# Optimization experiments

Measured on AMD Instinct MI355X. Metric: run time of the kernel, lower is better.

The kernel has to match this reference:

```python
import jax, jax.numpy as jnp
import numpy as np

HEADS = 4
HIDDEN = 128
NEG_SLOPE = 0.2
BN_EPS = 1e-5


def setup_inputs() -> dict:
    key = jax.random.key(0)
    ks = jax.random.split(key, 10)
    N, E, C, H = 10000, 320000, HIDDEN, HEADS
    D = C  # out_channels per head == hidden_channels
    glorot = lambda k, shape, fan: jax.random.normal(k, shape, dtype=jnp.float32) * np.float32(np.sqrt(2.0 / fan))
    x = jax.random.normal(ks[0], (N, C), dtype=jnp.float32)
    edge_index = jax.random.randint(ks[1], (2, E), 0, N, dtype=jnp.int64)
    W_l = glorot(ks[2], (C, H * D), C + H * D)
    b_l = jnp.zeros((H * D,), dtype=jnp.float32)
    W_r = glorot(ks[3], (C, H * D), C + H * D)
    b_r = jnp.zeros((H * D,), dtype=jnp.float32)
    att = glorot(ks[4], (H, D), D)
    bias = jnp.zeros((D,), dtype=jnp.float32)
    gamma = jnp.ones((D,), dtype=jnp.float32)
    beta = jnp.zeros((D,), dtype=jnp.float32)
    return {"x": x, "edge_index": edge_index, "W_l": W_l, "b_l": b_l,
            "W_r": W_r, "b_r": b_r, "att": att, "bias": bias,
            "gamma": gamma, "beta": beta}


def reference(x, edge_index, W_l, b_l, W_r, b_r, att, bias, gamma, beta):
    N, C = x.shape
    H = HEADS
    D = C
    # add self loops (PyG default add_self_loops=True)
    loops = jnp.arange(N, dtype=edge_index.dtype)
    src = jnp.concatenate([edge_index[0], loops])  # [E+N]
    dst = jnp.concatenate([edge_index[1], loops])  # [E+N]
    # GATv2: separate source/target transforms (share_weights=False)
    xl = (x @ W_l + b_l).reshape(N, H, D)  # source-side features
    xr = (x @ W_r + b_r).reshape(N, H, D)  # target-side features
    # per-edge score: a^T LeakyReLU(xl_j + xr_i)
    m = jax.nn.leaky_relu(xl[src] + xr[dst], negative_slope=NEG_SLOPE)  # [E',H,D]
    e = jnp.einsum('ehd,hd->eh', m, att)  # [E',H]
    # segment softmax over destination nodes
    emax = jax.ops.segment_max(e, dst, num_segments=N)  # [N,H]
    ee = jnp.exp(e - emax[dst])
    denom = jax.ops.segment_sum(ee, dst, num_segments=N)  # [N,H]
    alpha = ee / (denom[dst] + 1e-16)  # [E',H]
    # aggregate: sum_j alpha_ij * xl_j
    out = jax.ops.segment_sum(alpha[..., None] * xl[src], dst, num_segments=N)  # [N,H,D]
    out = out.mean(axis=1) + bias  # concat=False -> mean over heads, then bias
    # BatchNorm1d (training-mode batch statistics) + ReLU; dropout p=0
    mu = out.mean(axis=0)
    var = out.var(axis=0)
    out = gamma * (out - mu) * jax.lax.rsqrt(var + BN_EPS) + beta
    return jax.nn.relu(out)
```

## Files before the change

kernel.cpp:

```cpp
#include <hip/hip_runtime.h>
#include <math.h>

#define HEADS 4
#define HD 512
#define NEG 0.2f

typedef __attribute__((ext_vector_type(8))) short bf16x8;
typedef __attribute__((ext_vector_type(4))) float f32x4;

__device__ __forceinline__ unsigned short f2b(float f) {
    unsigned u = __float_as_uint(f);
    unsigned r = (u + 0x7fff + ((u >> 16) & 1)) >> 16;
    return (unsigned short)r;
}
__device__ __forceinline__ float lo16(unsigned u) { return __uint_as_float(u << 16); }
__device__ __forceinline__ float hi16(unsigned u) { return __uint_as_float(u & 0xffff0000u); }

__global__ __launch_bounds__(256) void prologue1(
    const float* __restrict__ Wl, const float* __restrict__ Wr,
    unsigned short* __restrict__ wlt, unsigned short* __restrict__ wrt,
    const int* __restrict__ ei, int E, int* __restrict__ deg,
    int* __restrict__ pos)
{
    const int bid = blockIdx.x;
    const int tid = threadIdx.x;
    if (bid < 128) {
        __shared__ float t[32][33];
        const int bx = bid & 15, by = (bid >> 4) & 3, bz = bid >> 6;
        const float* W = bz ? Wr : Wl;
        unsigned short* Wt = bz ? wrt : wlt;
        const int c0 = bx * 32, k0 = by * 32;
        {
            int k = tid >> 3, c4 = (tid & 7) * 4;
            float4 v = *(const float4*)(W + (size_t)(k0 + k) * 512 + c0 + c4);
            t[k][c4] = v.x; t[k][c4 + 1] = v.y; t[k][c4 + 2] = v.z; t[k][c4 + 3] = v.w;
        }
        __syncthreads();
        {
            int c = tid >> 3, k4 = (tid & 7) * 4;
            ushort4 o;
            o.x = f2b(t[k4][c]); o.y = f2b(t[k4 + 1][c]);
            o.z = f2b(t[k4 + 2][c]); o.w = f2b(t[k4 + 3][c]);
            *(ushort4*)(Wt + (size_t)(c0 + c) * 128 + k0 + k4) = o;
        }
    } else {
        int e = (bid - 128) * 256 + tid;
        if (e < E) pos[e] = atomicAdd(&deg[ei[E + e]], 1);
    }
}

__global__ __launch_bounds__(256) void scan_rowstart(
    const int* __restrict__ deg, int* __restrict__ rowstart, int N)
{
    __shared__ int ssum[256];
    int tid = threadIdx.x;
    int chunk = (N + 255) / 256;
    int start = tid * chunk;
    int end = min(start + chunk, N);
    int s = 0;
    for (int i = start; i < end; ++i) s += deg[i];
    ssum[tid] = s;
    __syncthreads();
    if (tid == 0) {
        int acc = 0;
        for (int i = 0; i < 256; ++i) { int t = ssum[i]; ssum[i] = acc; acc += t; }
    }
    __syncthreads();
    int acc = ssum[tid];
    for (int i = start; i < end; ++i) { rowstart[i] = acc; acc += deg[i]; }
    if (tid == 255) rowstart[N] = acc;
}

__global__ __launch_bounds__(256) void prologue2(
    const float* __restrict__ x,
    const unsigned short* __restrict__ wlt, const unsigned short* __restrict__ wrt,
    const float* __restrict__ bl, const float* __restrict__ br,
    unsigned short* __restrict__ xlb, unsigned short* __restrict__ xrb, int N,
    const int* __restrict__ ei, int E, const int* __restrict__ rowstart,
    const int* __restrict__ pos, int* __restrict__ adj)
{
    const int nrb = (N + 63) / 64;
    const int bid = blockIdx.x;
    if (bid >= nrb * 8) {
        int e = (bid - nrb * 8) * 256 + threadIdx.x;
        if (e < E) {
            int src = ei[e], dst = ei[E + e];
            adj[rowstart[dst] + pos[e]] = src;
        }
        return;
    }
    __shared__ float tile[4][16][132];

    const int bx = bid >> 3, by = bid & 7;
    const int wv = threadIdx.x >> 6;
    const int lane = threadIdx.x & 63;
    const int wsel = by >> 2;
    const int cb0 = (by & 3) * 128;
    const unsigned short* Wt = wsel ? wrt : wlt;
    const float* bias = wsel ? br : bl;
    unsigned short* out = wsel ? xrb : xlb;

    const int r0 = bx * 64 + wv * 16;
    const int row16 = lane & 15;
    const int kg = lane >> 4;
    int ar = r0 + row16;
    int arc = (ar < N) ? ar : (N - 1);
    const float* xrow = x + (size_t)arc * 128;

    f32x4 acc[8];
    #pragma unroll
    for (int i = 0; i < 8; ++i) acc[i] = (f32x4){0.f, 0.f, 0.f, 0.f};

    #pragma unroll
    for (int ks = 0; ks < 4; ++ks) {
        float4 f0 = *(const float4*)(xrow + ks * 32 + kg * 8);
        float4 f1 = *(const float4*)(xrow + ks * 32 + kg * 8 + 4);
        bf16x8 a;
        a[0] = f2b(f0.x); a[1] = f2b(f0.y); a[2] = f2b(f0.z); a[3] = f2b(f0.w);
        a[4] = f2b(f1.x); a[5] = f2b(f1.y); a[6] = f2b(f1.z); a[7] = f2b(f1.w);
        #pragma unroll
        for (int cb = 0; cb < 8; ++cb) {
            int col = cb0 + cb * 16 + row16;
            bf16x8 b = *(const bf16x8*)(Wt + (size_t)col * 128 + ks * 32 + kg * 8);
            acc[cb] = __builtin_amdgcn_mfma_f32_16x16x32_bf16(a, b, acc[cb], 0, 0, 0);
        }
    }

    #pragma unroll
    for (int cb = 0; cb < 8; ++cb) {
        int c = cb * 16 + row16;
        #pragma unroll
        for (int r = 0; r < 4; ++r)
            tile[wv][kg * 4 + r][c] = acc[cb][r];
    }
    __syncthreads();

    #pragma unroll
    for (int p = 0; p < 4; ++p) {
        int row = p * 4 + (lane >> 4);
        int grow = r0 + row;
        if (grow < N) {
            int c8 = (lane & 15) * 8;
            float4 b0v = *(const float4*)(bias + cb0 + c8);
            float4 b1v = *(const float4*)(bias + cb0 + c8 + 4);
            const float* tp = &tile[wv][row][c8];
            unsigned short t0 = f2b(tp[0] + b0v.x), t1 = f2b(tp[1] + b0v.y);
            unsigned short t2 = f2b(tp[2] + b0v.z), t3 = f2b(tp[3] + b0v.w);
            unsigned short t4 = f2b(tp[4] + b1v.x), t5 = f2b(tp[5] + b1v.y);
            unsigned short t6 = f2b(tp[6] + b1v.z), t7 = f2b(tp[7] + b1v.w);
            uint4 u;
            u.x = (unsigned)t0 | ((unsigned)t1 << 16);
            u.y = (unsigned)t2 | ((unsigned)t3 << 16);
            u.z = (unsigned)t4 | ((unsigned)t5 << 16);
            u.w = (unsigned)t6 | ((unsigned)t7 << 16);
            *(uint4*)(out + (size_t)grow * 512 + cb0 + c8) = u;
        }
    }
}

__global__ __launch_bounds__(256) void gat_aggr(
    const unsigned short* __restrict__ xlb, const unsigned short* __restrict__ xrb,
    const float* __restrict__ att, const float* __restrict__ bias,
    const int* __restrict__ rowstart, const int* __restrict__ adj,
    float* __restrict__ outm, int N)
{
    const int dst = blockIdx.x;
    const int wv = threadIdx.x >> 6;
    const int lane = threadIdx.x & 63;
    const int off = lane * 8;

    __shared__ float accs[4][64][9];

    uint4 ur = *(const uint4*)(xrb + (size_t)dst * HD + off);
    float xrv[8] = {lo16(ur.x), hi16(ur.x), lo16(ur.y), hi16(ur.y),
                    lo16(ur.z), hi16(ur.z), lo16(ur.w), hi16(ur.w)};
    const float4* pa = (const float4*)(att + off);
    float4 a0 = pa[0], a1 = pa[1];
    float av[8]  = {a0.x, a0.y, a0.z, a0.w, a1.x, a1.y, a1.z, a1.w};

    float dsum0 = 0.f, dsum1 = 0.f;
    float acc0[8] = {0.f, 0.f, 0.f, 0.f, 0.f, 0.f, 0.f, 0.f};
    float acc1[8] = {0.f, 0.f, 0.f, 0.f, 0.f, 0.f, 0.f, 0.f};

    auto proc = [&](int src, float& dsum, float* acc) {
        uint4 u = *(const uint4*)(xlb + (size_t)src * HD + off);
        float xlv[8] = {lo16(u.x), hi16(u.x), lo16(u.y), hi16(u.y),
                        lo16(u.z), hi16(u.z), lo16(u.w), hi16(u.w)};
        float s = 0.f;
        #pragma unroll
        for (int j = 0; j < 8; ++j) {
            float v = xlv[j] + xrv[j];
            s = fmaf(fmaxf(v, NEG * v), av[j], s);
        }
        s += __shfl_xor(s, 1, 64);
        s += __shfl_xor(s, 2, 64);
        s += __shfl_xor(s, 4, 64);
        s += __shfl_xor(s, 8, 64);
        float p = __expf(s);
        dsum += p;
        #pragma unroll
        for (int j = 0; j < 8; ++j) acc[j] = fmaf(p, xlv[j], acc[j]);
    };

    int beg = rowstart[dst];
    int deg = rowstart[dst + 1] - beg;
    int q = (deg + 3) >> 2;
    int b0 = beg + min(wv * q, deg);
    int e0 = beg + min((wv + 1) * q, deg);

    if (wv == 0) proc(dst, dsum0, acc0);
    int i = b0;
    for (; i + 1 < e0; i += 2) {
        int sA = adj[i], sB = adj[i + 1];
        proc(sA, dsum0, acc0);
        proc(sB, dsum1, acc1);
    }
    if (i < e0) proc(adj[i], dsum1, acc1);

    #pragma unroll
    for (int j = 0; j < 8; ++j) accs[wv][lane][j] = acc0[j] + acc1[j];
    accs[wv][lane][8] = dsum0 + dsum1;
    __syncthreads();

    if (wv == 0) {
        float A[8] = {0.f, 0.f, 0.f, 0.f, 0.f, 0.f, 0.f, 0.f};
        float D = 0.f;
        #pragma unroll
        for (int w = 0; w < 4; ++w) {
            #pragma unroll
            for (int j = 0; j < 8; ++j) A[j] += accs[w][lane][j];
            D += accs[w][lane][8];
        }
        float inv = 1.f / (D + 1e-16f);
        float vv[8];
        #pragma unroll
        for (int j = 0; j < 8; ++j) {
            float v = A[j] * inv;
            v += __shfl_xor(v, 16, 64);
            v += __shfl_xor(v, 32, 64);
            vv[j] = v;
        }
        if (lane < 16) {
            const float4* pb = (const float4*)(bias + lane * 8);
            float4 b0v = pb[0], b1v = pb[1];
            float4 o0 = make_float4(0.25f * vv[0] + b0v.x, 0.25f * vv[1] + b0v.y,
                                    0.25f * vv[2] + b0v.z, 0.25f * vv[3] + b0v.w);
            float4 o1 = make_float4(0.25f * vv[4] + b1v.x, 0.25f * vv[5] + b1v.y,
                                    0.25f * vv[6] + b1v.z, 0.25f * vv[7] + b1v.w);
            float4* po = (float4*)(outm + (size_t)dst * 128 + lane * 8);
            po[0] = o0; po[1] = o1;
        }
    }
}

__global__ __launch_bounds__(256) void bn_stats(
    const float* __restrict__ outm, float* __restrict__ musum,
    float* __restrict__ sqsum, int N)
{
    int tid = threadIdx.x;
    float s1 = 0.f, s2 = 0.f;
    size_t total = (size_t)N * 128;
    size_t stride = (size_t)gridDim.x * 256;
    for (size_t id = (size_t)blockIdx.x * 256 + tid; id < total; id += stride) {
        float v = outm[id];
        s1 += v; s2 += v * v;
    }
    __shared__ float sh1[256], sh2[256];
    sh1[tid] = s1; sh2[tid] = s2;
    __syncthreads();
    if (tid < 128) {
        atomicAdd(&musum[tid], sh1[tid] + sh1[tid + 128]);
        atomicAdd(&sqsum[tid], sh2[tid] + sh2[tid + 128]);
    }
}

__global__ __launch_bounds__(256) void finalize_b(
    float* __restrict__ outm, const float* __restrict__ musum,
    const float* __restrict__ sqsum, const float* __restrict__ gamma,
    const float* __restrict__ beta, int N)
{
    int id = blockIdx.x * 256 + threadIdx.x;
    if (id >= N * 128) return;
    int d = id & 127;
    float inv_n = 1.0f / (float)N;
    float mu = musum[d] * inv_n;
    float var = sqsum[d] * inv_n - mu * mu;
    float v = gamma[d] * (outm[id] - mu) * rsqrtf(var + 1e-5f) + beta[d];
    outm[id] = v > 0.f ? v : 0.f;
}

extern "C" void kernel_launch(void* const* d_in, const int* in_sizes, int n_in,
                              void* d_out, int out_size, void* d_ws, size_t ws_size,
                              hipStream_t stream) {
    const float* x     = (const float*)d_in[0];
    const int*   ei    = (const int*)d_in[1];
    const float* Wl    = (const float*)d_in[2];
    const float* bl    = (const float*)d_in[3];
    const float* Wr    = (const float*)d_in[4];
    const float* br    = (const float*)d_in[5];
    const float* att   = (const float*)d_in[6];
    const float* bias  = (const float*)d_in[7];
    const float* gamma = (const float*)d_in[8];
    const float* beta  = (const float*)d_in[9];

    const int N = in_sizes[0] / 128;
    const int E = in_sizes[1] / 2;

    unsigned short* xlb = (unsigned short*)d_ws;
    unsigned short* xrb = xlb + (size_t)N * 512;
    unsigned short* wlt = xrb + (size_t)N * 512;
    unsigned short* wrt = wlt + 65536;
    int*   deg      = (int*)(wrt + 65536);
    float* musum    = (float*)(deg + N);
    float* sqsum    = musum + 128;
    int*   rowstart = (int*)(sqsum + 128);
    int*   pos      = rowstart + (N + 1);
    int*   adj      = pos + E;
    float* outm     = (float*)d_out;

    hipMemsetAsync(deg, 0, ((size_t)N + 256) * sizeof(int), stream);

    int degBlocks = (E + 255) / 256;
    prologue1<<<128 + degBlocks, 256, 0, stream>>>(Wl, Wr, wlt, wrt, ei, E, deg, pos);

    scan_rowstart<<<1, 256, 0, stream>>>(deg, rowstart, N);

    int nrb = (N + 63) / 64;
    prologue2<<<nrb * 8 + degBlocks, 256, 0, stream>>>(
        x, wlt, wrt, bl, br, xlb, xrb, N, ei, E, rowstart, pos, adj);

    gat_aggr<<<N, 256, 0, stream>>>(xlb, xrb, att, bias, rowstart, adj, outm, N);

    bn_stats<<<512, 256, 0, stream>>>(outm, musum, sqsum, N);
    finalize_b<<<(N * 128 + 255) / 256, 256, 0, stream>>>(outm, musum, sqsum, gamma, beta, N);
}
```

Before: 147.4 us.

## Sort destinations by degree, pre-convert x to bf16, use packed float2 math

```diff
diff --git a/kernel.cpp b/kernel.cpp
--- a/kernel.cpp
+++ b/kernel.cpp
@@ -7,20 +7,35 @@
 
 typedef __attribute__((ext_vector_type(8))) short bf16x8;
 typedef __attribute__((ext_vector_type(4))) float f32x4;
+typedef __attribute__((ext_vector_type(2))) float f32x2;
 
 __device__ __forceinline__ unsigned short f2b(float f) {
     unsigned u = __float_as_uint(f);
     unsigned r = (u + 0x7fff + ((u >> 16) & 1)) >> 16;
     return (unsigned short)r;
 }
-__device__ __forceinline__ float lo16(unsigned u) { return __uint_as_float(u << 16); }
-__device__ __forceinline__ float hi16(unsigned u) { return __uint_as_float(u & 0xffff0000u); }
+__device__ __forceinline__ unsigned pack2(float a, float b) {
+    return (unsigned)f2b(a) | ((unsigned)f2b(b) << 16);
+}
+__device__ __forceinline__ f32x2 unpk(unsigned u) {
+    f32x2 r;
+    r.x = __uint_as_float(u << 16);
+    r.y = __uint_as_float(u & 0xffff0000u);
+    return r;
+}
+__device__ __forceinline__ f32x2 lrelu2(f32x2 v) {
+    f32x2 r;
+    r.x = fmaxf(v.x, NEG * v.x);
+    r.y = fmaxf(v.y, NEG * v.y);
+    return r;
+}
 
 __global__ __launch_bounds__(256) void prologue1(
     const float* __restrict__ Wl, const float* __restrict__ Wr,
     unsigned short* __restrict__ wlt, unsigned short* __restrict__ wrt,
+    const float* __restrict__ x, unsigned short* __restrict__ xb, int n8,
     const int* __restrict__ ei, int E, int* __restrict__ deg,
-    int* __restrict__ pos)
+    int* __restrict__ pos, int cvtxBlocks)
 {
     const int bid = blockIdx.x;
     const int tid = threadIdx.x;
@@ -43,16 +58,28 @@
             o.z = f2b(t[k4 + 2][c]); o.w = f2b(t[k4 + 3][c]);
             *(ushort4*)(Wt + (size_t)(c0 + c) * 128 + k0 + k4) = o;
         }
+    } else if (bid < 128 + cvtxBlocks) {
+        int i = (bid - 128) * 256 + tid;
+        if (i < n8) {
+            const float4* px = (const float4*)(x + (size_t)i * 8);
+            float4 f0 = px[0], f1 = px[1];
+            uint4 u;
+            u.x = pack2(f0.x, f0.y); u.y = pack2(f0.z, f0.w);
+            u.z = pack2(f1.x, f1.y); u.w = pack2(f1.z, f1.w);
+            ((uint4*)xb)[i] = u;
+        }
     } else {
-        int e = (bid - 128) * 256 + tid;
+        int e = (bid - 128 - cvtxBlocks) * 256 + tid;
         if (e < E) pos[e] = atomicAdd(&deg[ei[E + e]], 1);
     }
 }
 
 __global__ __launch_bounds__(256) void scan_rowstart(
-    const int* __restrict__ deg, int* __restrict__ rowstart, int N)
+    const int* __restrict__ deg, int* __restrict__ rowstart,
+    int* __restrict__ order, int N)
 {
     __shared__ int ssum[256];
+    __shared__ int bins[512];
     int tid = threadIdx.x;
     int chunk = (N + 255) / 256;
     int start = tid * chunk;
@@ -60,6 +87,7 @@
     int s = 0;
     for (int i = start; i < end; ++i) s += deg[i];
     ssum[tid] = s;
+    for (int i = tid; i < 512; i += 256) bins[i] = 0;
     __syncthreads();
     if (tid == 0) {
         int acc = 0;
@@ -67,12 +95,25 @@
     }
     __syncthreads();
     int acc = ssum[tid];
-    for (int i = start; i < end; ++i) { rowstart[i] = acc; acc += deg[i]; }
+    for (int i = start; i < end; ++i) {
+        rowstart[i] = acc; acc += deg[i];
+        atomicAdd(&bins[min(deg[i], 511)], 1);
+    }
     if (tid == 255) rowstart[N] = acc;
+    __syncthreads();
+    if (tid == 0) {
+        int a = 0;
+        for (int d = 511; d >= 0; --d) { int t = bins[d]; bins[d] = a; a += t; }
+    }
+    __syncthreads();
+    for (int i = start; i < end; ++i) {
+        int p = atomicAdd(&bins[min(deg[i], 511)], 1);
+        order[p] = i;
+    }
 }
 
 __global__ __launch_bounds__(256) void prologue2(
-    const float* __restrict__ x,
+    const unsigned short* __restrict__ xb,
     const unsigned short* __restrict__ wlt, const unsigned short* __restrict__ wrt,
     const float* __restrict__ bl, const float* __restrict__ br,
     unsigned short* __restrict__ xlb, unsigned short* __restrict__ xrb, int N,
@@ -105,7 +146,7 @@
     const int kg = lane >> 4;
     int ar = r0 + row16;
     int arc = (ar < N) ? ar : (N - 1);
-    const float* xrow = x + (size_t)arc * 128;
+    const unsigned short* xrow = xb + (size_t)arc * 128;
 
     f32x4 acc[8];
     #pragma unroll
@@ -113,11 +154,7 @@
 
     #pragma unroll
     for (int ks = 0; ks < 4; ++ks) {
-        float4 f0 = *(const float4*)(xrow + ks * 32 + kg * 8);
-        float4 f1 = *(const float4*)(xrow + ks * 32 + kg * 8 + 4);
-        bf16x8 a;
-        a[0] = f2b(f0.x); a[1] = f2b(f0.y); a[2] = f2b(f0.z); a[3] = f2b(f0.w);
-        a[4] = f2b(f1.x); a[5] = f2b(f1.y); a[6] = f2b(f1.z); a[7] = f2b(f1.w);
+        bf16x8 a = *(const bf16x8*)(xrow + ks * 32 + kg * 8);
         #pragma unroll
         for (int cb = 0; cb < 8; ++cb) {
             int col = cb0 + cb * 16 + row16;
@@ -144,15 +181,11 @@
             float4 b0v = *(const float4*)(bias + cb0 + c8);
             float4 b1v = *(const float4*)(bias + cb0 + c8 + 4);
             const float* tp = &tile[wv][row][c8];
-            unsigned short t0 = f2b(tp[0] + b0v.x), t1 = f2b(tp[1] + b0v.y);
-            unsigned short t2 = f2b(tp[2] + b0v.z), t3 = f2b(tp[3] + b0v.w);
-            unsigned short t4 = f2b(tp[4] + b1v.x), t5 = f2b(tp[5] + b1v.y);
-            unsigned short t6 = f2b(tp[6] + b1v.z), t7 = f2b(tp[7] + b1v.w);
             uint4 u;
-            u.x = (unsigned)t0 | ((unsigned)t1 << 16);
-            u.y = (unsigned)t2 | ((unsigned)t3 << 16);
-            u.z = (unsigned)t4 | ((unsigned)t5 << 16);
-            u.w = (unsigned)t6 | ((unsigned)t7 << 16);
+            u.x = pack2(tp[0] + b0v.x, tp[1] + b0v.y);
+            u.y = pack2(tp[2] + b0v.z, tp[3] + b0v.w);
+            u.z = pack2(tp[4] + b1v.x, tp[5] + b1v.y);
+            u.w = pack2(tp[6] + b1v.z, tp[7] + b1v.w);
             *(uint4*)(out + (size_t)grow * 512 + cb0 + c8) = u;
         }
     }
@@ -162,9 +195,9 @@
     const unsigned short* __restrict__ xlb, const unsigned short* __restrict__ xrb,
     const float* __restrict__ att, const float* __restrict__ bias,
     const int* __restrict__ rowstart, const int* __restrict__ adj,
-    float* __restrict__ outm, int N)
-{
-    const int dst = blockIdx.x;
+    const int* __restrict__ order, float* __restrict__ outm, int N)
+{
+    const int dst = order[blockIdx.x];
     const int wv = threadIdx.x >> 6;
     const int lane = threadIdx.x & 63;
     const int off = lane * 8;
@@ -172,34 +205,35 @@
     __shared__ float accs[4][64][9];
 
     uint4 ur = *(const uint4*)(xrb + (size_t)dst * HD + off);
-    float xrv[8] = {lo16(ur.x), hi16(ur.x), lo16(ur.y), hi16(ur.y),
-                    lo16(ur.z), hi16(ur.z), lo16(ur.w), hi16(ur.w)};
+    f32x2 xr0 = unpk(ur.x), xr1 = unpk(ur.y), xr2 = unpk(ur.z), xr3 = unpk(ur.w);
     const float4* pa = (const float4*)(att + off);
     float4 a0 = pa[0], a1 = pa[1];
-    float av[8]  = {a0.x, a0.y, a0.z, a0.w, a1.x, a1.y, a1.z, a1.w};
+    f32x2 av0 = {a0.x, a0.y}, av1 = {a0.z, a0.w};
+    f32x2 av2 = {a1.x, a1.y}, av3 = {a1.z, a1.w};
 
     float dsum0 = 0.f, dsum1 = 0.f;
-    float acc0[8] = {0.f, 0.f, 0.f, 0.f, 0.f, 0.f, 0.f, 0.f};
-    float acc1[8] = {0.f, 0.f, 0.f, 0.f, 0.f, 0.f, 0.f, 0.f};
-
-    auto proc = [&](int src, float& dsum, float* acc) {
+    f32x2 acc0[4] = {{0.f,0.f},{0.f,0.f},{0.f,0.f},{0.f,0.f}};
+    f32x2 acc1[4] = {{0.f,0.f},{0.f,0.f},{0.f,0.f},{0.f,0.f}};
+
+    auto proc = [&](int src, float& dsum, f32x2* acc) {
         uint4 u = *(const uint4*)(xlb + (size_t)src * HD + off);
-        float xlv[8] = {lo16(u.x), hi16(u.x), lo16(u.y), hi16(u.y),
-                        lo16(u.z), hi16(u.z), lo16(u.w), hi16(u.w)};
-        float s = 0.f;
-        #pragma unroll
-        for (int j = 0; j < 8; ++j) {
-            float v = xlv[j] + xrv[j];
-            s = fmaf(fmaxf(v, NEG * v), av[j], s);
-        }
+        f32x2 l0 = unpk(u.x), l1 = unpk(u.y), l2 = unpk(u.z), l3 = unpk(u.w);
+        f32x2 s2 = lrelu2(l0 + xr0) * av0;
+        s2 += lrelu2(l1 + xr1) * av1;
+        s2 += lrelu2(l2 + xr2) * av2;
+        s2 += lrelu2(l3 + xr3) * av3;
+        float s = s2.x + s2.y;
         s += __shfl_xor(s, 1, 64);
         s += __shfl_xor(s, 2, 64);
         s += __shfl_xor(s, 4, 64);
         s += __shfl_xor(s, 8, 64);
         float p = __expf(s);
         dsum += p;
-        #pragma unroll
-        for (int j = 0; j < 8; ++j) acc[j] = fmaf(p, xlv[j], acc[j]);
+        f32x2 p2 = {p, p};
+        acc[0] += p2 * l0;
+        acc[1] += p2 * l1;
+        acc[2] += p2 * l2;
+        acc[3] += p2 * l3;
     };
 
     int beg = rowstart[dst];
@@ -208,7 +242,7 @@
     int b0 = beg + min(wv * q, deg);
     int e0 = beg + min((wv + 1) * q, deg);
 
-    if (wv == 0) proc(dst, dsum0, acc0);
+    if (wv == 3) proc(dst, dsum0, acc0);
     int i = b0;
     for (; i + 1 < e0; i += 2) {
         int sA = adj[i], sB = adj[i + 1];
@@ -218,7 +252,11 @@
     if (i < e0) proc(adj[i], dsum1, acc1);
 
     #pragma unroll
-    for (int j = 0; j < 8; ++j) accs[wv][lane][j] = acc0[j] + acc1[j];
+    for (int j = 0; j < 4; ++j) {
+        f32x2 t = acc0[j] + acc1[j];
+        accs[wv][lane][2 * j]     = t.x;
+        accs[wv][lane][2 * j + 1] = t.y;
+    }
     accs[wv][lane][8] = dsum0 + dsum1;
     __syncthreads();
 
@@ -308,7 +346,8 @@
 
     unsigned short* xlb = (unsigned short*)d_ws;
     unsigned short* xrb = xlb + (size_t)N * 512;
-    unsigned short* wlt = xrb + (size_t)N * 512;
+    unsigned short* xb  = xrb + (size_t)N * 512;
+    unsigned short* wlt = xb + (size_t)N * 128;
     unsigned short* wrt = wlt + 65536;
     int*   deg      = (int*)(wrt + 65536);
     float* musum    = (float*)(deg + N);
@@ -316,20 +355,24 @@
     int*   rowstart = (int*)(sqsum + 128);
     int*   pos      = rowstart + (N + 1);
     int*   adj      = pos + E;
+    int*   order    = adj + E;
     float* outm     = (float*)d_out;
 
     hipMemsetAsync(deg, 0, ((size_t)N + 256) * sizeof(int), stream);
 
+    int n8 = N * 128 / 8;
+    int cvtxBlocks = (n8 + 255) / 256;
     int degBlocks = (E + 255) / 256;
-    prologue1<<<128 + degBlocks, 256, 0, stream>>>(Wl, Wr, wlt, wrt, ei, E, deg, pos);
-
-    scan_rowstart<<<1, 256, 0, stream>>>(deg, rowstart, N);
+    prologue1<<<128 + cvtxBlocks + degBlocks, 256, 0, stream>>>(
+        Wl, Wr, wlt, wrt, x, xb, n8, ei, E, deg, pos, cvtxBlocks);
+
+    scan_rowstart<<<1, 256, 0, stream>>>(deg, rowstart, order, N);
 
     int nrb = (N + 63) / 64;
     prologue2<<<nrb * 8 + degBlocks, 256, 0, stream>>>(
-        x, wlt, wrt, bl, br, xlb, xrb, N, ei, E, rowstart, pos, adj);
-
-    gat_aggr<<<N, 256, 0, stream>>>(xlb, xrb, att, bias, rowstart, adj, outm, N);
+        xb, wlt, wrt, bl, br, xlb, xrb, N, ei, E, rowstart, pos, adj);
+
+    gat_aggr<<<N, 256, 0, stream>>>(xlb, xrb, att, bias, rowstart, adj, order, outm, N);
 
     bn_stats<<<512, 256, 0, stream>>>(outm, musum, sqsum, N);
     finalize_b<<<(N * 128 + 255) / 256, 256, 0, stream>>>(outm, musum, sqsum, gamma, beta, N);
```

Measured after the change: 165.4 us. 1.12x slower.
